# Kernel optimization log

Measured on AMD Instinct MI355X. Metric: run time of the kernel, lower is better.

## Reference

```python
import jax, jax.numpy as jnp
import numpy as np

B, S, D, H, DM = 2, 2048, 1024, 16, 4
HD = D // H  # head_dim = 64
EPS = 1e-5


def setup_inputs() -> dict:
    key = jax.random.key(0)
    ks = jax.random.split(key, 8)
    s = 0.02
    return {
        "x": jax.random.normal(ks[0], (B, S, D), jnp.float32),
        "wq": jax.random.normal(ks[1], (D, D), jnp.float32) * s,
        "wk": jax.random.normal(ks[2], (D, D), jnp.float32) * s,
        "wv": jax.random.normal(ks[3], (D, D), jnp.float32) * s,
        "wo": jax.random.normal(ks[4], (D, D), jnp.float32) * s,
        "bo": jnp.zeros((D,), jnp.float32),
        "ln1_scale": jnp.ones((D,), jnp.float32),
        "ln1_shift": jnp.zeros((D,), jnp.float32),
        "ln2_scale": jnp.ones((D,), jnp.float32),
        "ln2_shift": jnp.zeros((D,), jnp.float32),
        "w1": jax.random.normal(ks[5], (DM * D, D), jnp.float32) * s,
        "b1": jnp.zeros((DM * D,), jnp.float32),
        "w2": jax.random.normal(ks[6], (D, DM * D), jnp.float32) * s,
        "b2": jnp.zeros((D,), jnp.float32),
    }


def _layernorm(x, scale, shift):
    mean = jnp.mean(x, axis=-1, keepdims=True)
    var = jnp.var(x, axis=-1, keepdims=True)  # unbiased=False
    return scale * (x - mean) * jax.lax.rsqrt(var + EPS) + shift


def _attn(x, wq, wk, wv, wo, bo):
    b, n, d = x.shape
    # torch Linear: y = x @ W.T
    q = (x @ wq.T).reshape(b, n, H, HD).transpose(0, 2, 1, 3)  # [b,h,n,hd]
    k = (x @ wk.T).reshape(b, n, H, HD).transpose(0, 2, 1, 3)
    v = (x @ wv.T).reshape(b, n, H, HD).transpose(0, 2, 1, 3)
    scores = jnp.einsum("bhqd,bhkd->bhqk", q, k)
    causal = jnp.tril(jnp.ones((n, n), bool))
    scores = jnp.where(causal, scores, -jnp.inf)
    w = jax.nn.softmax(scores / np.sqrt(HD).astype(np.float32), axis=-1)
    ctx = jnp.einsum("bhqk,bhkd->bhqd", w, v)
    ctx = ctx.transpose(0, 2, 1, 3).reshape(b, n, d)
    return ctx @ wo.T + bo


def reference(x, wq, wk, wv, wo, bo, ln1_scale, ln1_shift, ln2_scale, ln2_shift, w1, b1, w2, b2):
    h = x + _attn(_layernorm(x, ln1_scale, ln1_shift), wq, wk, wv, wo, bo)
    y = _layernorm(h, ln2_scale, ln2_shift)
    y = jax.nn.relu(y @ w1.T + b1) @ w2.T + b2
    return h + y
```

## Files before the change

### kernel.cpp

```cpp
#include <hip/hip_runtime.h>
#include <hip/hip_bf16.h>

#define DEV __device__ __forceinline__

typedef __attribute__((ext_vector_type(8))) short bf8;
typedef __attribute__((ext_vector_type(4))) float f4;
typedef __attribute__((ext_vector_type(16))) float f16x;

#define GLOAD_LDS(gp, lp) \
  __builtin_amdgcn_global_load_lds( \
      (const __attribute__((address_space(1))) void*)(gp), \
      (__attribute__((address_space(3))) void*)(lp), 16, 0, 0)

DEV unsigned short f2bf(float f) {
  union { __hip_bfloat16 h; unsigned short u; } c;
  c.h = __float2bfloat16(f);
  return c.u;
}
DEV unsigned int pk2(float a, float b) {
  union { __hip_bfloat162 h; unsigned int u; } c;
  c.h = __hip_bfloat162(__float2bfloat16(a), __float2bfloat16(b));
  return c.u;
}

DEV int2 swz_tile(int ob, int nxt, int nyt) {
  const int nb = nxt * nyt;
  const int cpx = nb >> 3;
  const int W = (ob & 7) * cpx + (ob >> 3);
  const int scw = 4 * nyt;
  const int sc = W / scw, rem = W - sc * scw;
  return make_int2(rem >> 2, sc * 4 + (rem & 3));
}

template<bool BIAS, bool RELU, bool RESID, bool OUTBF, bool WRVT>
__global__ __launch_bounds__(256) void gemm_bt128(
    const unsigned short* __restrict__ A, const unsigned short* __restrict__ B,
    const float* __restrict__ bias, const float* __restrict__ resid,
    void* __restrict__ Cout, int M, int N, int K, int ldc,
    unsigned short* __restrict__ vtout, int nyt)
{
  __shared__ unsigned short Al[2][128 * 32];
  __shared__ unsigned short Bl[2][128 * 32];
  const int t = threadIdx.x;
  const int w = t >> 6, l = t & 63;
  const int wr = w >> 1, wc = w & 1;
  int2 tt = swz_tile((int)blockIdx.x, N >> 7, nyt);
  const int m0 = tt.x * 128, n0 = tt.y * 128;

  const int srow = w * 16 + (l >> 2);
  const int scsw = ((l & 3) * 8) ^ (((srow >> 1) & 3) << 3);
  const unsigned short* Ab = A + (size_t)(m0 + srow) * K + scsw;
  const unsigned short* Bb = B + (size_t)(n0 + srow) * K + scsw;
  const int sdst = w * 512 + l * 8;

  auto STAGE = [&](int slot, int k0) {
#pragma unroll
    for (int i = 0; i < 2; ++i) {
      GLOAD_LDS(Ab + (size_t)i * 64 * K + k0, &Al[slot][sdst + i * 2048]);
      GLOAD_LDS(Bb + (size_t)i * 64 * K + k0, &Bl[slot][sdst + i * 2048]);
    }
  };

  const f4 fz = {0.f, 0.f, 0.f, 0.f};
  f4 acc[4][4];
#pragma unroll
  for (int i = 0; i < 4; ++i)
#pragma unroll
    for (int j = 0; j < 4; ++j) acc[i][j] = fz;

  const int NT = K >> 5;
  STAGE(0, 0);
  __syncthreads();

  for (int T = 0; T < NT; ++T) {
    if (T + 1 < NT) STAGE((T + 1) & 1, (T + 1) * 32);
    const int sl = T & 1;
    const int rdcol = ((l >> 4) * 8) ^ ((((l & 15) >> 1) & 3) << 3);
    bf8 af[4], bg[4];
#pragma unroll
    for (int am = 0; am < 4; ++am)
      af[am] = *(const bf8*)&Al[sl][(wr * 64 + am * 16 + (l & 15)) * 32 + rdcol];
#pragma unroll
    for (int bn = 0; bn < 4; ++bn)
      bg[bn] = *(const bf8*)&Bl[sl][(wc * 64 + bn * 16 + (l & 15)) * 32 + rdcol];
    __builtin_amdgcn_s_setprio(1);
#pragma unroll
    for (int am = 0; am < 4; ++am)
#pragma unroll
      for (int bn = 0; bn < 4; ++bn)
        acc[am][bn] = __builtin_amdgcn_mfma_f32_16x16x32_bf16(af[am], bg[bn], acc[am][bn], 0, 0, 0);
    __builtin_amdgcn_s_setprio(0);
    __syncthreads();
  }

#pragma unroll
  for (int bn = 0; bn < 4; ++bn) {
    const int col = n0 + wc * 64 + bn * 16 + (l & 15);
    float bv = 0.f;
    if (BIAS) bv = bias[col];
    const bool isv = WRVT && (col >= 2048);
    const int hh = (col - 2048) >> 6, dd = (col - 2048) & 63;
#pragma unroll
    for (int am = 0; am < 4; ++am) {
#pragma unroll
      for (int r = 0; r < 4; ++r) {
        const int row = m0 + wr * 64 + am * 16 + ((l >> 4) * 4) + r;
        float v = acc[am][bn][r] + bv;
        if (RELU) v = fmaxf(v, 0.f);
        if (RESID) v += resid[(size_t)row * ldc + col];
        if (WRVT && isv) {
          const int bb = row >> 11, ss = row & 2047;
          vtout[((size_t)(bb * 16 + hh) * 64 + dd) * 2048 + ss] = f2bf(v);
        } else if (OUTBF) {
          ((unsigned short*)Cout)[(size_t)row * ldc + col] = f2bf(v);
        } else {
          ((float*)Cout)[(size_t)row * ldc + col] = v;
        }
      }
    }
  }
}

template<bool BIAS, bool RELU, bool RESID, bool OUTBF>
__global__ __launch_bounds__(256) void gemm_bt64(
    const unsigned short* __restrict__ A, const unsigned short* __restrict__ B,
    const float* __restrict__ bias, const float* __restrict__ resid,
    void* __restrict__ Cout, int M, int N, int K, int ldc)
{
  __shared__ unsigned short Al[2][64 * 64];
  __shared__ unsigned short Bl[2][128 * 64];
  const int t = threadIdx.x;
  const int w = t >> 6, l = t & 63;
  const int wr = w >> 1, wc = w & 1;
  int2 tt = swz_tile((int)blockIdx.x, N >> 7, M >> 6);
  const int m0 = tt.x * 64, n0 = tt.y * 128;

  const int srow = t >> 3;
  const int scol = 8 * ((t & 7) ^ (srow & 7));
  const unsigned short* Ab = A + (size_t)(m0 + srow) * K + scol;
  const unsigned short* Bb = B + (size_t)(n0 + srow) * K + scol;
  const int sdst = srow * 64 + (t & 7) * 8;

  auto STAGE = [&](int slot, int k0) {
#pragma unroll
    for (int i = 0; i < 2; ++i)
      GLOAD_LDS(Ab + (size_t)(i * 32) * K + k0, &Al[slot][sdst + i * 32 * 64]);
#pragma unroll
    for (int i = 0; i < 4; ++i)
      GLOAD_LDS(Bb + (size_t)(i * 32) * K + k0, &Bl[slot][sdst + i * 32 * 64]);
  };

  const f4 fz = {0.f, 0.f, 0.f, 0.f};
  f4 acc[2][4];
#pragma unroll
  for (int i = 0; i < 2; ++i)
#pragma unroll
    for (int j = 0; j < 4; ++j) acc[i][j] = fz;

  const int NT = K >> 6;
  STAGE(0, 0);
  __syncthreads();

  for (int T = 0; T < NT; ++T) {
    if (T + 1 < NT) STAGE((T + 1) & 1, (T + 1) * 64);
    const int sl = T & 1;
#pragma unroll
    for (int ks = 0; ks < 2; ++ks) {
      const int cb = (ks * 64 + ((l >> 4) * 16)) ^ ((l & 7) << 4);
      bf8 af[2], bg[4];
#pragma unroll
      for (int am = 0; am < 2; ++am)
        af[am] = *(const bf8*)((const char*)&Al[sl][(wr * 32 + am * 16 + (l & 15)) * 64] + cb);
#pragma unroll
      for (int bn = 0; bn < 4; ++bn)
        bg[bn] = *(const bf8*)((const char*)&Bl[sl][(wc * 64 + bn * 16 + (l & 15)) * 64] + cb);
      __builtin_amdgcn_s_setprio(1);
#pragma unroll
      for (int am = 0; am < 2; ++am)
#pragma unroll
        for (int bn = 0; bn < 4; ++bn)
          acc[am][bn] = __builtin_amdgcn_mfma_f32_16x16x32_bf16(af[am], bg[bn], acc[am][bn], 0, 0, 0);
      __builtin_amdgcn_s_setprio(0);
    }
    __syncthreads();
  }

#pragma unroll
  for (int bn = 0; bn < 4; ++bn) {
    const int col = n0 + wc * 64 + bn * 16 + (l & 15);
    float bv = 0.f;
    if (BIAS) bv = bias[col];
#pragma unroll
    for (int am = 0; am < 2; ++am) {
#pragma unroll
      for (int r = 0; r < 4; ++r) {
        const int row = m0 + wr * 32 + am * 16 + ((l >> 4) * 4) + r;
        float v = acc[am][bn][r] + bv;
        if (RELU) v = fmaxf(v, 0.f);
        if (RESID) v += resid[(size_t)row * ldc + col];
        if (OUTBF) ((unsigned short*)Cout)[(size_t)row * ldc + col] = f2bf(v);
        else       ((float*)Cout)[(size_t)row * ldc + col] = v;
      }
    }
  }
}

__global__ __launch_bounds__(256, 4) void attn_kernel(
    const unsigned short* __restrict__ qk, const unsigned short* __restrict__ vt,
    unsigned short* __restrict__ ctx)
{
  __shared__ unsigned short SM[2][2][64 * 64];

  const int t = threadIdx.x;
  const int w = t >> 6, l = t & 63;
  const int p = w >> 1;
  const int hi = l >> 5, q = l & 31;
  const int bid = blockIdx.x;
  const int xcd = bid & 7, i = bid >> 3;
  const int g = i >> 5, c = i & 31;
  const int s = (g & 1) ? c : 31 - c;
  const int bh = xcd * 4 + g;
  const int b = bh >> 4, h = bh & 15;
  const int tile = 2 * s + (w & 1);
  const int q0w = tile * 32;
  const int h0 = (s + 2) >> 1;

  const unsigned short* qbase = qk + ((size_t)b * 2048) * 2048 + h * 64;
  const unsigned short* kbase = qbase + 1024;
  const unsigned short* vbase = vt + (size_t)bh * 64 * 2048;
  unsigned short* Kl = &SM[p][0][0];
  unsigned short* Vl = &SM[p][1][0];
  const int tp = t & 127;

  bf8 qf[4];
#pragma unroll
  for (int ksl = 0; ksl < 4; ++ksl)
    qf[ksl] = *(const bf8*)(qbase + (size_t)(q0w + q) * 2048 + ksl * 16 + hi * 8);

  f16x oacc[2];
#pragma unroll
  for (int dn = 0; dn < 2; ++dn)
#pragma unroll
    for (int i2 = 0; i2 < 16; ++i2) oacc[dn][i2] = 0.f;
  float m_ = -1e30f, l_ = 0.f;

  for (int it = 0; it < h0; ++it) {
    const int gi = p ? h0 + it : it;
    const bool act = gi <= s;
    __syncthreads();
    if (act) {
#pragma unroll
      for (int ss = 0; ss < 4; ++ss) {
        const int row = ss * 16 + (tp >> 3);
        const int cb = (tp & 7) * 16;
        const int sb = cb ^ ((row & 7) << 4);
        GLOAD_LDS(kbase + (size_t)(gi * 64 + row) * 2048 + (sb >> 1),
                  &Kl[row * 64 + (cb >> 1)]);
        GLOAD_LDS(vbase + (size_t)row * 2048 + gi * 64 + (sb >> 1),
                  &Vl[row * 64 + (cb >> 1)]);
      }
    }
    __syncthreads();
    if (act) {
      const int kb0 = gi * 64;

      f16x s0, s1;
#pragma unroll
      for (int i2 = 0; i2 < 16; ++i2) { s0[i2] = 0.f; s1[i2] = 0.f; }
      __builtin_amdgcn_s_setprio(1);
#pragma unroll
      for (int ksl = 0; ksl < 4; ++ksl) {
        const int cbq = (ksl * 16 + hi * 8) * 2;
        const int r0 = q, r1 = 32 + q;
        bf8 k0 = *(const bf8*)((const char*)&Kl[r0 * 64] + (cbq ^ ((r0 & 7) << 4)));
        bf8 k1 = *(const bf8*)((const char*)&Kl[r1 * 64] + (cbq ^ ((r1 & 7) << 4)));
        s0 = __builtin_amdgcn_mfma_f32_32x32x16_bf16(k0, qf[ksl], s0, 0, 0, 0);
        s1 = __builtin_amdgcn_mfma_f32_32x32x16_bf16(k1, qf[ksl], s1, 0, 0, 0);
      }
      __builtin_amdgcn_s_setprio(0);

      float pv[32];
      if (gi == s) {
#pragma unroll
        for (int i2 = 0; i2 < 16; ++i2) {
          const int key = kb0 + (i2 & 3) + 8 * (i2 >> 2) + 4 * hi;
          pv[i2]      = (key <= q0w + q)      ? s0[i2] : -1e30f;
          pv[16 + i2] = (key + 32 <= q0w + q) ? s1[i2] : -1e30f;
        }
      } else {
#pragma unroll
        for (int i2 = 0; i2 < 16; ++i2) { pv[i2] = s0[i2]; pv[16 + i2] = s1[i2]; }
      }

      float tm[16];
#pragma unroll
      for (int i2 = 0; i2 < 16; ++i2) tm[i2] = fmaxf(pv[i2], pv[16 + i2]);
#pragma unroll
      for (int st = 8; st >= 1; st >>= 1)
#pragma unroll
        for (int i2 = 0; i2 < 8; ++i2)
          if (i2 < st) tm[i2] = fmaxf(tm[i2], tm[i2 + st]);
      const float pmax = fmaxf(tm[0], __shfl_xor(tm[0], 32));
      if (__any(pmax > m_ + 11.54f)) {
        const float mn = fmaxf(m_, pmax);
        const float alpha = __builtin_amdgcn_exp2f(m_ - mn);
        m_ = mn;
        l_ *= alpha;
#pragma unroll
        for (int dn = 0; dn < 2; ++dn)
#pragma unroll
          for (int i2 = 0; i2 < 16; ++i2) oacc[dn][i2] *= alpha;
      }
#pragma unroll
      for (int i2 = 0; i2 < 32; ++i2) pv[i2] = __builtin_amdgcn_exp2f(pv[i2] - m_);
      float ts[16];
#pragma unroll
      for (int i2 = 0; i2 < 16; ++i2) ts[i2] = pv[i2] + pv[16 + i2];
#pragma unroll
      for (int st = 8; st >= 1; st >>= 1)
#pragma unroll
        for (int i2 = 0; i2 < 8; ++i2)
          if (i2 < st) ts[i2] += ts[i2 + st];
      l_ += ts[0] + __shfl_xor(ts[0], 32);

#pragma unroll
      for (int sg = 0; sg < 2; ++sg) {
        const float* pp = pv + sg * 16;
        unsigned int wds[8];
#pragma unroll
        for (int m = 0; m < 4; ++m) {
          wds[m * 2]     = pk2(pp[4 * m], pp[4 * m + 1]);
          wds[m * 2 + 1] = pk2(pp[4 * m + 2], pp[4 * m + 3]);
        }
#pragma unroll
        for (int kq = 0; kq < 2; ++kq) {
          unsigned int x0 = __shfl_xor((int)(hi ? wds[4 * kq]     : wds[4 * kq + 2]), 32);
          unsigned int x1 = __shfl_xor((int)(hi ? wds[4 * kq + 1] : wds[4 * kq + 3]), 32);
          union { unsigned int u[4]; bf8 v; } pu;
          pu.u[0] = hi ? x0 : wds[4 * kq];
          pu.u[1] = hi ? x1 : wds[4 * kq + 1];
          pu.u[2] = hi ? wds[4 * kq + 2] : x0;
          pu.u[3] = hi ? wds[4 * kq + 3] : x1;
          const bf8 pf = pu.v;
          __builtin_amdgcn_s_setprio(1);
#pragma unroll
          for (int dn = 0; dn < 2; ++dn) {
            const int row = dn * 32 + q;
            const int cb = ((sg * 32 + kq * 16 + hi * 8) * 2) ^ ((row & 7) << 4);
            bf8 vf = *(const bf8*)((const char*)&Vl[row * 64] + cb);
            oacc[dn] = __builtin_amdgcn_mfma_f32_32x32x16_bf16(vf, pf, oacc[dn], 0, 0, 0);
          }
          __builtin_amdgcn_s_setprio(0);
        }
      }
    }
  }

  __syncthreads();
  float* mb = (float*)&SM[0][0][0];
  if (p == 1) {
    float* base = mb + (w & 1) * 2176;
    base[l] = m_;
    base[64 + l] = l_;
#pragma unroll
    for (int dn = 0; dn < 2; ++dn)
#pragma unroll
      for (int i2 = 0; i2 < 16; ++i2)
        base[128 + (dn * 16 + i2) * 64 + l] = oacc[dn][i2];
  }
  __syncthreads();
  if (p == 0) {
    float* base = mb + (w & 1) * 2176;
    const float m2 = base[l], l2 = base[64 + l];
    const float mm = fmaxf(m_, m2);
    const float a0 = __builtin_amdgcn_exp2f(m_ - mm);
    const float a2 = __builtin_amdgcn_exp2f(m2 - mm);
    const float inv = 1.0f / (a0 * l_ + a2 * l2);
    unsigned short* crow = ctx + ((size_t)(b * 2048 + q0w + q)) * 1024 + h * 64;
#pragma unroll
    for (int dn = 0; dn < 2; ++dn)
#pragma unroll
      for (int m = 0; m < 4; ++m) {
        float o0 = a0 * oacc[dn][4 * m]     + a2 * base[128 + (dn * 16 + 4 * m) * 64 + l];
        float o1 = a0 * oacc[dn][4 * m + 1] + a2 * base[128 + (dn * 16 + 4 * m + 1) * 64 + l];
        float o2 = a0 * oacc[dn][4 * m + 2] + a2 * base[128 + (dn * 16 + 4 * m + 2) * 64 + l];
        float o3 = a0 * oacc[dn][4 * m + 3] + a2 * base[128 + (dn * 16 + 4 * m + 3) * 64 + l];
        const int d0 = dn * 32 + 8 * m + 4 * hi;
        *(unsigned int*)(crow + d0)     = pk2(o0 * inv, o1 * inv);
        *(unsigned int*)(crow + d0 + 2) = pk2(o2 * inv, o3 * inv);
      }
  }
}

__global__ __launch_bounds__(256) void ln_kernel(
    const float* __restrict__ x, const float* __restrict__ sc,
    const float* __restrict__ sh, unsigned short* __restrict__ out)
{
  const int row = blockIdx.x, t = threadIdx.x;
  float4 v = ((const float4*)x)[(size_t)row * 256 + t];
  float s = v.x + v.y + v.z + v.w;
  float q = v.x * v.x + v.y * v.y + v.z * v.z + v.w * v.w;
#pragma unroll
  for (int off = 1; off < 64; off <<= 1) {
    s += __shfl_xor(s, off);
    q += __shfl_xor(q, off);
  }
  __shared__ float red[8];
  const int w = t >> 6, l = t & 63;
  if (l == 0) { red[w] = s; red[4 + w] = q; }
  __syncthreads();
  s = red[0] + red[1] + red[2] + red[3];
  q = red[4] + red[5] + red[6] + red[7];
  const float mean = s * (1.0f / 1024.0f);
  const float var = q * (1.0f / 1024.0f) - mean * mean;
  const float rstd = rsqrtf(var + 1e-5f);
  float4 scv = ((const float4*)sc)[t];
  float4 shv = ((const float4*)sh)[t];
  uint2 p;
  p.x = pk2(scv.x * (v.x - mean) * rstd + shv.x, scv.y * (v.y - mean) * rstd + shv.y);
  p.y = pk2(scv.z * (v.z - mean) * rstd + shv.z, scv.w * (v.w - mean) * rstd + shv.w);
  ((uint2*)out)[(size_t)row * 256 + t] = p;
}

__global__ __launch_bounds__(256) void cvt_weights(
    const float* __restrict__ wq, const float* __restrict__ wk,
    const float* __restrict__ wv, const float* __restrict__ wo,
    const float* __restrict__ w1, const float* __restrict__ w2,
    unsigned short* __restrict__ dst)
{
  const int M1 = 1 << 20;
  const int n4 = (12 * M1) / 4;
  const int stride = gridDim.x * 256;
  for (int i4 = blockIdx.x * 256 + threadIdx.x; i4 < n4; i4 += stride) {
    const size_t i = (size_t)i4 * 4;
    const int mi = (int)(i >> 20);
    const float* src;
    size_t off;
    float sc = 1.0f;
    if (mi < 4) {
      src = mi == 0 ? wq : mi == 1 ? wk : mi == 2 ? wv : wo;
      off = i & (size_t)(M1 - 1);
      if (mi == 0) sc = 0.125f * 1.44269504088896f;
    } else if (mi < 8) {
      src = w1; off = i - (size_t)4 * M1;
    } else {
      src = w2; off = i - (size_t)8 * M1;
    }
    float4 v = *(const float4*)(src + off);
    uint2 pq;
    pq.x = pk2(v.x * sc, v.y * sc);
    pq.y = pk2(v.z * sc, v.w * sc);
    ((uint2*)dst)[i4] = pq;
  }
}

extern "C" void kernel_launch(void* const* d_in, const int* in_sizes, int n_in,
                              void* d_out, int out_size, void* d_ws, size_t ws_size,
                              hipStream_t stream)
{
  const float* x    = (const float*)d_in[0];
  const float* wq   = (const float*)d_in[1];
  const float* wk   = (const float*)d_in[2];
  const float* wv   = (const float*)d_in[3];
  const float* wo   = (const float*)d_in[4];
  const float* bo   = (const float*)d_in[5];
  const float* ln1s = (const float*)d_in[6];
  const float* ln1b = (const float*)d_in[7];
  const float* ln2s = (const float*)d_in[8];
  const float* ln2b = (const float*)d_in[9];
  const float* w1   = (const float*)d_in[10];
  const float* b1   = (const float*)d_in[11];
  const float* w2   = (const float*)d_in[12];
  const float* b2   = (const float*)d_in[13];
  float* out = (float*)d_out;

  const int M = 4096;

  unsigned short* ws   = (unsigned short*)d_ws;
  unsigned short* lnb  = ws;
  unsigned short* qkvw = lnb  + (size_t)4096 * 1024;
  unsigned short* wob  = qkvw + (size_t)3072 * 1024;
  unsigned short* w1b  = wob  + (size_t)1024 * 1024;
  unsigned short* w2b  = w1b  + (size_t)4096 * 1024;
  unsigned short* qkb  = w2b  + (size_t)4096 * 1024;
  unsigned short* vtb  = qkb  + (size_t)4096 * 2048;
  unsigned short* ctxb = vtb  + (size_t)32 * 64 * 2048;
  float* hf = (float*)(ctxb + (size_t)4096 * 1024);

  cvt_weights<<<2048, 256, 0, stream>>>(wq, wk, wv, wo, w1, w2, qkvw);

  ln_kernel<<<M, 256, 0, stream>>>(x, ln1s, ln1b, lnb);
  gemm_bt128<false, false, false, true, true><<<768, 256, 0, stream>>>(
      lnb, qkvw, nullptr, nullptr, qkb, M, 3072, 1024, 2048, vtb, 32);
  attn_kernel<<<1024, 256, 0, stream>>>(qkb, vtb, ctxb);
  gemm_bt64<true, false, true, false><<<512, 256, 0, stream>>>(
      ctxb, wob, bo, x, hf, M, 1024, 1024, 1024);
  ln_kernel<<<M, 256, 0, stream>>>(hf, ln2s, ln2b, lnb);
  gemm_bt128<true, true, false, true, false><<<1024, 256, 0, stream>>>(
      lnb, w1b, b1, nullptr, qkb, M, 4096, 1024, 4096, nullptr, 32);
  gemm_bt64<true, false, true, false><<<512, 256, 0, stream>>>(
      qkb, w2b, b2, hf, out, M, 1024, 4096, 1024);
}
```

Before: 236.2 us.

## Split-K the FFN down-projection GEMM into two halves with a reduction kernel

The final FFN2 GEMM (K=4096) is split along K into two halves, doubling the grid from 512 to 1024 blocks. Each half writes fp32 partial sums, one into reused workspace and one into the output buffer. A separate reduce kernel then adds the residual, both partials and the bias. This aims to improve CU occupancy on the long-K GEMM, at the cost of extra fp32 partial traffic (about 16MB each) and one more kernel launch.

New measurement: 242.4 us. 2.6% more time.

```diff
diff --git a/kernel.cpp b/kernel.cpp
--- a/kernel.cpp
+++ b/kernel.cpp
@@ -202,6 +202,100 @@
         else       ((float*)Cout)[(size_t)row * ldc + col] = v;
       }
     }
+  }
+}
+
+__global__ __launch_bounds__(256) void gemm_bt64_sk(
+    const unsigned short* __restrict__ A, const unsigned short* __restrict__ B,
+    float* __restrict__ p0, float* __restrict__ p1,
+    int M, int N, int Kstride, int klen)
+{
+  __shared__ unsigned short Al[2][64 * 32];
+  __shared__ unsigned short Bl[2][128 * 32];
+  const int t = threadIdx.x;
+  const int w = t >> 6, l = t & 63;
+  const int wr = w >> 1, wc = w & 1;
+  const int kh = (int)blockIdx.x & 1;
+  const int koff = kh * klen;
+  int2 tt = swz_tile((int)blockIdx.x >> 1, N >> 7, M >> 6);
+  const int m0 = tt.x * 64, n0 = tt.y * 128;
+  float* pout = kh ? p1 : p0;
+
+  const int srow = w * 16 + (l >> 2);
+  const int scsw = ((l & 3) * 8) ^ (((srow >> 1) & 3) << 3);
+  const unsigned short* Ab = A + (size_t)(m0 + srow) * Kstride + koff + scsw;
+  const unsigned short* Bb = B + (size_t)(n0 + srow) * Kstride + koff + scsw;
+  const int sdst = w * 512 + l * 8;
+
+  auto STAGE = [&](int slot, int k0) {
+    GLOAD_LDS(Ab + k0, &Al[slot][sdst]);
+#pragma unroll
+    for (int i = 0; i < 2; ++i)
+      GLOAD_LDS(Bb + (size_t)i * 64 * Kstride + k0, &Bl[slot][sdst + i * 2048]);
+  };
+
+  const f4 fz = {0.f, 0.f, 0.f, 0.f};
+  f4 acc[2][4];
+#pragma unroll
+  for (int i = 0; i < 2; ++i)
+#pragma unroll
+    for (int j = 0; j < 4; ++j) acc[i][j] = fz;
+
+  const int NT = klen >> 5;
+  STAGE(0, 0);
+  __syncthreads();
+
+  for (int T = 0; T < NT; ++T) {
+    if (T + 1 < NT) STAGE((T + 1) & 1, (T + 1) * 32);
+    const int sl = T & 1;
+    const int rdcol = ((l >> 4) * 8) ^ ((((l & 15) >> 1) & 3) << 3);
+    bf8 af[2], bg[4];
+#pragma unroll
+    for (int am = 0; am < 2; ++am)
+      af[am] = *(const bf8*)&Al[sl][(wr * 32 + am * 16 + (l & 15)) * 32 + rdcol];
+#pragma unroll
+    for (int bn = 0; bn < 4; ++bn)
+      bg[bn] = *(const bf8*)&Bl[sl][(wc * 64 + bn * 16 + (l & 15)) * 32 + rdcol];
+    __builtin_amdgcn_s_setprio(1);
+#pragma unroll
+    for (int am = 0; am < 2; ++am)
+#pragma unroll
+      for (int bn = 0; bn < 4; ++bn)
+        acc[am][bn] = __builtin_amdgcn_mfma_f32_16x16x32_bf16(af[am], bg[bn], acc[am][bn], 0, 0, 0);
+    __builtin_amdgcn_s_setprio(0);
+    __syncthreads();
+  }
+
+#pragma unroll
+  for (int bn = 0; bn < 4; ++bn) {
+    const int col = n0 + wc * 64 + bn * 16 + (l & 15);
+#pragma unroll
+    for (int am = 0; am < 2; ++am) {
+#pragma unroll
+      for (int r = 0; r < 4; ++r) {
+        const int row = m0 + wr * 32 + am * 16 + ((l >> 4) * 4) + r;
+        pout[(size_t)row * N + col] = acc[am][bn][r];
+      }
+    }
+  }
+}
+
+__global__ __launch_bounds__(256) void reduce_ffn2(
+    const float* __restrict__ hf, const float* __restrict__ p0,
+    const float* __restrict__ b2, float* __restrict__ out, int n4)
+{
+  const int stride = gridDim.x * 256;
+  for (int i = blockIdx.x * 256 + threadIdx.x; i < n4; i += stride) {
+    float4 a = ((const float4*)hf)[i];
+    float4 b = ((const float4*)p0)[i];
+    float4 c = ((const float4*)out)[i];
+    float4 d = ((const float4*)b2)[i & 255];
+    float4 o;
+    o.x = a.x + b.x + c.x + d.x;
+    o.y = a.y + b.y + c.y + d.y;
+    o.z = a.z + b.z + c.z + d.z;
+    o.w = a.w + b.w + c.w + d.w;
+    ((float4*)out)[i] = o;
   }
 }
 
@@ -486,6 +580,7 @@
   unsigned short* vtb  = qkb  + (size_t)4096 * 2048;
   unsigned short* ctxb = vtb  + (size_t)32 * 64 * 2048;
   float* hf = (float*)(ctxb + (size_t)4096 * 1024);
+  float* p0 = (float*)lnb;
 
   cvt_weights<<<2048, 256, 0, stream>>>(wq, wk, wv, wo, w1, w2, qkvw);
 
@@ -498,6 +593,6 @@
   ln_kernel<<<M, 256, 0, stream>>>(hf, ln2s, ln2b, lnb);
   gemm_bt128<true, true, false, true, false><<<1024, 256, 0, stream>>>(
       lnb, w1b, b1, nullptr, qkb, M, 4096, 1024, 4096, nullptr, 32);
-  gemm_bt64<true, false, true, false><<<512, 256, 0, stream>>>(
-      qkb, w2b, b2, hf, out, M, 1024, 4096, 1024);
-}
+  gemm_bt64_sk<<<1024, 256, 0, stream>>>(qkb, w2b, p0, out, M, 1024, 4096, 2048);
+  reduce_ffn2<<<2048, 256, 0, stream>>>(hf, p0, b2, out, (M * 1024) / 4);
+}
```
